# Optimization experiments

Hardware: AMD Instinct MI355X
Metric: run time of the kernel (lower is better)

The kernel has to match this reference:

```python
import jax, jax.numpy as jnp
import numpy as np

N_HEADS = 8; N_LEVELS = 4; T_WINDOW = 2; N_CURR = 4; N_TEMP = 2; D_MODEL = 256
D_HEAD = D_MODEL // N_HEADS
SHAPES = [[4, 32, 48], [4, 16, 24], [4, 8, 12], [4, 4, 6]]  # (T, H, W) per level
LEN_IN = sum(t * h * w for t, h, w in SHAPES)  # 8160
LEN_Q = LEN_IN
N_BATCH = 1


def _bilinear_sample(value_l, loc):
    # value_l: (N, M, H, W, D); loc: (N, M, Q, P, 2) normalized to [0, 1].
    # Matches torch grid_sample(mode='bilinear', padding_mode='zeros', align_corners=False)
    # with grid = 2*loc - 1, i.e. pixel coords x = loc_x*W - 0.5, y = loc_y*H - 0.5.
    N, M, H, W, D = value_l.shape
    Q, P = loc.shape[2], loc.shape[3]
    x = loc[..., 0] * W - 0.5
    y = loc[..., 1] * H - 0.5
    x0 = jnp.floor(x); y0 = jnp.floor(y)
    wx = x - x0; wy = y - y0
    flat = value_l.reshape(N, M, H * W, D)

    def gather(xi, yi):
        valid = ((xi >= 0) & (xi < W) & (yi >= 0) & (yi < H)).astype(value_l.dtype)
        idx = (jnp.clip(yi, 0, H - 1) * W + jnp.clip(xi, 0, W - 1)).astype(jnp.int32)
        g = jnp.take_along_axis(flat, idx.reshape(N, M, Q * P, 1), axis=2)
        return g.reshape(N, M, Q, P, D) * valid[..., None]

    v00 = gather(x0, y0); v10 = gather(x0 + 1.0, y0)
    v01 = gather(x0, y0 + 1.0); v11 = gather(x0 + 1.0, y0 + 1.0)
    return (v00 * ((1 - wx) * (1 - wy))[..., None] + v10 * (wx * (1 - wy))[..., None]
            + v01 * ((1 - wx) * wy)[..., None] + v11 * (wx * wy)[..., None])


def _forward(query, reference_points, temporal_offsets, input_flatten, shapes, starts,
             Wv, bv, Ws, bs, Wa, ba, Wts, bts, Wta, bta, Wo, bo):
    N, Lq, _ = query.shape
    value = (input_flatten @ Wv + bv).reshape(N, -1, N_HEADS, D_HEAD)
    ts_off = (query @ Wts + bts).reshape(N, Lq, N_HEADS, N_LEVELS, T_WINDOW, N_TEMP, 2)
    t_attn = (query @ Wta + bta).reshape(N, Lq, N_HEADS, N_LEVELS * T_WINDOW * N_TEMP)
    c_attn = (query @ Wa + ba).reshape(N, Lq, N_HEADS, N_LEVELS * N_CURR)
    # joint softmax over current + temporal sampling points (as in the source)
    attn = jax.nn.softmax(jnp.concatenate([c_attn, t_attn], axis=-1), axis=-1)
    aw_c = attn[..., :N_LEVELS * N_CURR].reshape(N, Lq, N_HEADS, N_LEVELS, N_CURR)
    aw_t = attn[..., N_LEVELS * N_CURR:].reshape(N, Lq, N_HEADS, N_LEVELS, T_WINDOW * N_TEMP)
    aw = jnp.concatenate([aw_c, aw_t], axis=4)  # (N, Lq, M, L, P)
    c_off = (query @ Ws + bs).reshape(N, Lq, N_HEADS, N_LEVELS, N_CURR, 2)
    # flattened-temporal grid per level: width W_l, height T_l*H_l
    norm = jnp.array([[w, t * h] for t, h, w in shapes], dtype=query.dtype)  # (L, 2)
    loc_c = reference_points[:, :, None, :, None, :] + c_off / norm[None, None, None, :, None, :]
    loc_t = (reference_points[:, :, None, :, None, None, :]
             + temporal_offsets[:, :, None, :, :, None, :]
             + ts_off / norm[None, None, None, :, None, None, :])
    loc_t = loc_t.reshape(N, Lq, N_HEADS, N_LEVELS, T_WINDOW * N_TEMP, 2)
    locs = jnp.concatenate([loc_c, loc_t], axis=4)  # (N, Lq, M, L, P, 2)
    out = jnp.zeros((N, N_HEADS, Lq, D_HEAD), query.dtype)
    for l, (t, h, w) in enumerate(shapes):
        s = starts[l]
        vl = value[:, s:s + t * h * w].transpose(0, 2, 1, 3).reshape(N, N_HEADS, t * h, w, D_HEAD)
        loc_l = locs[:, :, :, l].transpose(0, 2, 1, 3, 4)   # (N, M, Lq, P, 2)
        sampled = _bilinear_sample(vl, loc_l)               # (N, M, Lq, P, Dh)
        w_l = aw[:, :, :, l].transpose(0, 2, 1, 3)          # (N, M, Lq, P)
        out = out + jnp.einsum('nmqpd,nmqp->nmqd', sampled, w_l)
    out = out.transpose(0, 2, 1, 3).reshape(N, Lq, D_MODEL)
    return out @ Wo + bo


def setup_inputs() -> dict:
    key = jax.random.key(0)
    ks = jax.random.split(key, 18)
    D = D_MODEL
    sc = 0.02
    query = jax.random.normal(ks[0], (N_BATCH, LEN_Q, D), jnp.float32)
    reference_points = jax.random.uniform(ks[1], (N_BATCH, LEN_Q, N_LEVELS, 2), jnp.float32)
    temporal_offsets = jax.random.uniform(ks[2], (N_BATCH, LEN_Q, N_LEVELS, T_WINDOW, 2),
                                          jnp.float32, minval=-0.25, maxval=0.25)
    input_flatten = jax.random.normal(ks[3], (N_BATCH, LEN_IN, D), jnp.float32)
    input_spatial_shapes = jnp.array(SHAPES, dtype=jnp.int32)
    starts = np.cumsum([0] + [t * h * w for t, h, w in SHAPES])[:-1]
    input_level_start_index = jnp.array(starts, dtype=jnp.int32)
    n_off = N_HEADS * N_LEVELS * N_CURR * 2          # 256
    n_att = N_HEADS * N_LEVELS * N_CURR              # 128
    n_toff = N_HEADS * N_LEVELS * T_WINDOW * N_TEMP * 2  # 256
    n_tatt = N_HEADS * N_LEVELS * T_WINDOW * N_TEMP      # 128
    return {
        'query': query, 'reference_points': reference_points,
        'temporal_offsets': temporal_offsets, 'input_flatten': input_flatten,
        'input_spatial_shapes': input_spatial_shapes,
        'input_level_start_index': input_level_start_index,
        'Wv': jax.random.normal(ks[4], (D, D), jnp.float32) * sc,
        'bv': jnp.zeros((D,), jnp.float32),
        'Ws': jax.random.normal(ks[5], (D, n_off), jnp.float32) * sc,
        'bs': jax.random.normal(ks[6], (n_off,), jnp.float32) * 2.0,
        'Wa': jax.random.normal(ks[7], (D, n_att), jnp.float32) * sc,
        'ba': jnp.zeros((n_att,), jnp.float32),
        'Wts': jax.random.normal(ks[8], (D, n_toff), jnp.float32) * sc,
        'bts': jax.random.normal(ks[9], (n_toff,), jnp.float32) * 2.0,
        'Wta': jax.random.normal(ks[10], (D, n_tatt), jnp.float32) * sc,
        'bta': jnp.zeros((n_tatt,), jnp.float32),
        'Wo': jax.random.normal(ks[11], (D, D), jnp.float32) * sc,
        'bo': jnp.zeros((D,), jnp.float32),
    }


def reference(query, reference_points, temporal_offsets, input_flatten,
              input_spatial_shapes, input_level_start_index,
              Wv, bv, Ws, bs, Wa, ba, Wts, bts, Wta, bta, Wo, bo):
    shapes = [tuple(int(v) for v in row) for row in np.asarray(input_spatial_shapes)]
    starts = [int(v) for v in np.asarray(input_level_start_index)]
    return _forward(query, reference_points, temporal_offsets, input_flatten,
                    shapes, starts, Wv, bv, Ws, bs, Wa, ba, Wts, bts, Wta, bta, Wo, bo)
```

## Files before the change

kernel.cpp:

```cpp
#include <hip/hip_runtime.h>


#define LEN 8160
#define NCONV8 (2 * LEN * 256 / 8)
#define NPACK8 (1280 * 256 / 8)

typedef __attribute__((ext_vector_type(8))) short bf16x8;
typedef __attribute__((ext_vector_type(8))) unsigned short u16x8;
typedef __attribute__((ext_vector_type(4))) float f32x4;

__device__ __forceinline__ unsigned short rne_bf16(float v)
{
    unsigned u = __float_as_uint(v);
    return (unsigned short)((u + 0x7FFFu + ((u >> 16) & 1u)) >> 16);
}

__device__ __forceinline__ void split_bf16(float v, unsigned short* hi, unsigned short* lo)
{
    unsigned u = __float_as_uint(v);
    unsigned r = (u + 0x7FFFu + ((u >> 16) & 1u)) & 0xFFFF0000u;
    float hif = __uint_as_float(r);
    float lof = v - hif;
    unsigned ul = __float_as_uint(lof);
    unsigned rl = (ul + 0x7FFFu + ((ul >> 16) & 1u)) >> 16;
    *hi = (unsigned short)(r >> 16);
    *lo = (unsigned short)rl;
}

__device__ __forceinline__ float bf2f(unsigned short s)
{
    return __uint_as_float(((unsigned)s) << 16);
}

__global__ __launch_bounds__(256) void prep_kernel(
    const float* __restrict__ inpf, const float* __restrict__ query,
    const float* __restrict__ Ws, const float* __restrict__ bs,
    const float* __restrict__ Wa, const float* __restrict__ ba,
    const float* __restrict__ Wts, const float* __restrict__ bts,
    const float* __restrict__ Wta, const float* __restrict__ bta,
    const float* __restrict__ Wv, const float* __restrict__ Wo,
    unsigned short* __restrict__ Ahi, unsigned short* __restrict__ Alo,
    unsigned short* __restrict__ Qhi, unsigned short* __restrict__ Qlo,
    unsigned short* __restrict__ Whi, unsigned short* __restrict__ Wlo,
    float* __restrict__ bcat)
{
    int idx = blockIdx.x * 256 + threadIdx.x;
    if (idx < NCONV8) {
        int which = (idx >= NCONV8 / 2) ? 1 : 0;
        int off = (idx - which * (NCONV8 / 2)) * 8;
        const float* src = which ? query : inpf;
        float4 a = *(const float4*)(src + off);
        float4 b = *(const float4*)(src + off + 4);
        unsigned short h[8], l[8];
        split_bf16(a.x, &h[0], &l[0]); split_bf16(a.y, &h[1], &l[1]);
        split_bf16(a.z, &h[2], &l[2]); split_bf16(a.w, &h[3], &l[3]);
        split_bf16(b.x, &h[4], &l[4]); split_bf16(b.y, &h[5], &l[5]);
        split_bf16(b.z, &h[6], &l[6]); split_bf16(b.w, &h[7], &l[7]);
        uint4 hv, lv;
        hv.x = h[0] | ((unsigned)h[1] << 16); hv.y = h[2] | ((unsigned)h[3] << 16);
        hv.z = h[4] | ((unsigned)h[5] << 16); hv.w = h[6] | ((unsigned)h[7] << 16);
        lv.x = l[0] | ((unsigned)l[1] << 16); lv.y = l[2] | ((unsigned)l[3] << 16);
        lv.z = l[4] | ((unsigned)l[5] << 16); lv.w = l[6] | ((unsigned)l[7] << 16);
        if (which) { *(uint4*)(Qhi + off) = hv; *(uint4*)(Qlo + off) = lv; }
        else       { *(uint4*)(Ahi + off) = hv; *(uint4*)(Alo + off) = lv; }
    } else if (idx < NCONV8 + NPACK8) {
        int j8 = idx - NCONV8;
        int n = j8 >> 5;
        int k0 = (j8 & 31) << 3;
        unsigned short h[8], l[8];
        #pragma unroll
        for (int t = 0; t < 8; t++) {
            int k = k0 + t;
            float v;
            if (n < 256) v = Wv[k * 256 + n];
            else if (n < 1024) {
                int j = n - 256;
                if (j < 256)      v = Ws [k * 256 + j];
                else if (j < 384) v = Wa [k * 128 + (j - 256)];
                else if (j < 640) v = Wts[k * 256 + (j - 384)];
                else              v = Wta[k * 128 + (j - 640)];
            } else v = Wo[k * 256 + (n - 1024)];
            split_bf16(v, &h[t], &l[t]);
        }
        uint4 hv, lv;
        hv.x = h[0] | ((unsigned)h[1] << 16); hv.y = h[2] | ((unsigned)h[3] << 16);
        hv.z = h[4] | ((unsigned)h[5] << 16); hv.w = h[6] | ((unsigned)h[7] << 16);
        lv.x = l[0] | ((unsigned)l[1] << 16); lv.y = l[2] | ((unsigned)l[3] << 16);
        lv.z = l[4] | ((unsigned)l[5] << 16); lv.w = l[6] | ((unsigned)l[7] << 16);
        *(uint4*)(Whi + n * 256 + k0) = hv;
        *(uint4*)(Wlo + n * 256 + k0) = lv;
    } else if (idx < NCONV8 + NPACK8 + 768) {
        int j = idx - (NCONV8 + NPACK8);
        float v;
        if (j < 256)      v = bs[j];
        else if (j < 384) v = ba[j - 256];
        else if (j < 640) v = bts[j - 384];
        else              v = bta[j - 640];
        bcat[j] = v;
    }
}

__global__ __launch_bounds__(512) void gemm_mfma_dual(
    const unsigned short* __restrict__ A0hi, const unsigned short* __restrict__ A0lo,
    const unsigned short* __restrict__ B0hi, const unsigned short* __restrict__ B0lo,
    const float* __restrict__ bias0, void* __restrict__ C0, int N0, int mode0, int nbx0,
    const unsigned short* __restrict__ A1hi, const unsigned short* __restrict__ A1lo,
    const unsigned short* __restrict__ B1hi, const unsigned short* __restrict__ B1lo,
    const float* __restrict__ bias1, void* __restrict__ C1, int N1, int mode1)
{
    __shared__ unsigned short Bf[2 * 8 * 4 * 64 * 8];
    const int tid = threadIdx.x;
    const int wave = tid >> 6, lane = tid & 63;
    int bx = blockIdx.x;
    const int by = blockIdx.y;

    const unsigned short *Ahi, *Alo, *Bhi, *Blo;
    const float* bias; void* C; int N, mode;
    if (bx < nbx0) {
        Ahi = A0hi; Alo = A0lo; Bhi = B0hi; Blo = B0lo;
        bias = bias0; C = C0; N = N0; mode = mode0;
    } else {
        bx -= nbx0;
        Ahi = A1hi; Alo = A1lo; Bhi = B1hi; Blo = B1lo;
        bias = bias1; C = C1; N = N1; mode = mode1;
    }

    #pragma unroll
    for (int t = 0; t < 8; t++) {
        int f = t * 512 + tid;
        int ln = f & 63, nt = (f >> 6) & 3, kt = (f >> 8) & 7, pl = f >> 11;
        const unsigned short* src = (pl ? Blo : Bhi)
            + (size_t)(bx * 64 + nt * 16 + (ln & 15)) * 256 + kt * 32 + (ln >> 4) * 8;
        *(uint4*)(&Bf[(size_t)f * 8]) = *(const uint4*)src;
    }
    __syncthreads();

    const int lm = lane & 15;
    const int kq = lane >> 4;
    const int m0 = by * 256 + wave * 32 + lm;
    const unsigned short* aH0 = Ahi + (size_t)m0 * 256 + kq * 8;
    const unsigned short* aL0 = Alo + (size_t)m0 * 256 + kq * 8;

    f32x4 acc[2][4] = {};
    #pragma unroll
    for (int kt = 0; kt < 8; kt++) {
        bf16x8 ah0 = *(const bf16x8*)(aH0 + kt * 32);
        bf16x8 al0 = *(const bf16x8*)(aL0 + kt * 32);
        bf16x8 ah1 = *(const bf16x8*)(aH0 + 16 * 256 + kt * 32);
        bf16x8 al1 = *(const bf16x8*)(aL0 + 16 * 256 + kt * 32);
        #pragma unroll
        for (int nt = 0; nt < 4; nt++) {
            const int fb = (kt * 4 + nt) * 64 + lane;
            bf16x8 bh = *(const bf16x8*)(&Bf[(size_t)fb * 8]);
            bf16x8 bl = *(const bf16x8*)(&Bf[(size_t)(fb + 2048) * 8]);
            acc[0][nt] = __builtin_amdgcn_mfma_f32_16x16x32_bf16(ah0, bh, acc[0][nt], 0, 0, 0);
            acc[0][nt] = __builtin_amdgcn_mfma_f32_16x16x32_bf16(ah0, bl, acc[0][nt], 0, 0, 0);
            acc[0][nt] = __builtin_amdgcn_mfma_f32_16x16x32_bf16(al0, bh, acc[0][nt], 0, 0, 0);
            acc[1][nt] = __builtin_amdgcn_mfma_f32_16x16x32_bf16(ah1, bh, acc[1][nt], 0, 0, 0);
            acc[1][nt] = __builtin_amdgcn_mfma_f32_16x16x32_bf16(ah1, bl, acc[1][nt], 0, 0, 0);
            acc[1][nt] = __builtin_amdgcn_mfma_f32_16x16x32_bf16(al1, bh, acc[1][nt], 0, 0, 0);
        }
    }

    const int col = bx * 64 + lm;
    #pragma unroll
    for (int sub = 0; sub < 2; sub++) {
        const int row0 = by * 256 + wave * 32 + sub * 16 + kq * 4;
        #pragma unroll
        for (int nt = 0; nt < 4; nt++) {
            float bb = bias[col + nt * 16];
            #pragma unroll
            for (int r = 0; r < 4; r++) {
                int row = row0 + r;
                if (row < LEN) {
                    float v = acc[sub][nt][r] + bb;
                    if (mode) ((unsigned short*)C)[(size_t)row * N + col + nt * 16] = rne_bf16(v);
                    else      ((float*)C)[(size_t)row * N + col + nt * 16] = v;
                }
            }
        }
    }
}

__global__ __launch_bounds__(256) void sample_kernel(
    const unsigned short* __restrict__ value,
    const float* __restrict__ proj,
    const float* __restrict__ refp,
    const float* __restrict__ toff,
    unsigned short* __restrict__ attn_hi,
    unsigned short* __restrict__ attn_lo)
{
    const int q = blockIdx.x;
    const int head = threadIdx.x >> 5;
    const int lane = threadIdx.x & 31;
    __shared__ int4   s_idx[8][32];
    __shared__ float4 s_w[8][32];

    const float* p = proj + (size_t)q * 768;

    {
        const int i = lane;
        float logit, ox, oy, rx, ry;
        int l;
        if (i < 16) {
            l = i >> 2; int pt2 = i & 3;
            logit = p[256 + head * 16 + i];
            ox = p[head * 32 + l * 8 + pt2 * 2 + 0];
            oy = p[head * 32 + l * 8 + pt2 * 2 + 1];
            rx = refp[q * 8 + l * 2 + 0];
            ry = refp[q * 8 + l * 2 + 1];
        } else {
            int j = i - 16; l = j >> 2;
            int tp = j & 3, tw = tp >> 1, nt = tp & 1;
            logit = p[640 + head * 16 + j];
            ox = p[384 + head * 32 + l * 8 + tw * 4 + nt * 2 + 0];
            oy = p[384 + head * 32 + l * 8 + tw * 4 + nt * 2 + 1];
            rx = refp[q * 8 + l * 2 + 0] + toff[q * 16 + l * 4 + tw * 2 + 0];
            ry = refp[q * 8 + l * 2 + 1] + toff[q * 16 + l * 4 + tw * 2 + 1];
        }
        const int Wl = 48 >> l;
        const int Hgl = 128 >> l;
        const int st = 8192 - (8192 >> (2 * l));
        const float fW = (float)Wl, fHg = (float)Hgl;
        float x = (rx + ox / fW) * fW - 0.5f;
        float y = (ry + oy / fHg) * fHg - 0.5f;

        float mx = logit;
        #pragma unroll
        for (int off = 16; off > 0; off >>= 1)
            mx = fmaxf(mx, __shfl_xor(mx, off, 32));
        float e = expf(logit - mx);
        float s = e;
        #pragma unroll
        for (int off = 16; off > 0; off >>= 1)
            s += __shfl_xor(s, off, 32);
        float w = e / s;

        float fx = floorf(x), fy = floorf(y);
        float wx = x - fx, wy = y - fy;
        int x0 = (int)fx, y0 = (int)fy;
        int x1 = x0 + 1, y1 = y0 + 1;
        float m00 = ((unsigned)x0 < (unsigned)Wl && (unsigned)y0 < (unsigned)Hgl) ? 1.f : 0.f;
        float m10 = ((unsigned)x1 < (unsigned)Wl && (unsigned)y0 < (unsigned)Hgl) ? 1.f : 0.f;
        float m01 = ((unsigned)x0 < (unsigned)Wl && (unsigned)y1 < (unsigned)Hgl) ? 1.f : 0.f;
        float m11 = ((unsigned)x1 < (unsigned)Wl && (unsigned)y1 < (unsigned)Hgl) ? 1.f : 0.f;
        int cx0 = min(max(x0, 0), Wl - 1), cx1 = min(max(x1, 0), Wl - 1);
        int cy0 = min(max(y0, 0), Hgl - 1), cy1 = min(max(y1, 0), Hgl - 1);
        int4 ii;
        ii.x = (st + cy0 * Wl + cx0) * 512;
        ii.y = (st + cy0 * Wl + cx1) * 512;
        ii.z = (st + cy1 * Wl + cx0) * 512;
        ii.w = (st + cy1 * Wl + cx1) * 512;
        float sx0 = 1.f - wx, sy0 = 1.f - wy;
        float4 ww;
        ww.x = w * sx0 * sy0 * m00;
        ww.y = w * wx  * sy0 * m10;
        ww.z = w * sx0 * wy  * m01;
        ww.w = w * wx  * wy  * m11;
        s_idx[head][lane] = ii;
        s_w[head][lane] = ww;
    }
    __syncthreads();

    const int pt8 = lane >> 2;
    const int cg  = lane & 3;
    const char* vbase = (const char*)value + head * 64 + cg * 16;
    float acc[8] = {0.f, 0.f, 0.f, 0.f, 0.f, 0.f, 0.f, 0.f};
    #pragma unroll
    for (int i = 0; i < 4; i++) {
        int pidx = (i << 3) | pt8;
        int4 ii = s_idx[head][pidx];
        float4 ww = s_w[head][pidx];
        u16x8 v0 = *(const u16x8*)(vbase + ii.x);
        u16x8 v1 = *(const u16x8*)(vbase + ii.y);
        u16x8 v2 = *(const u16x8*)(vbase + ii.z);
        u16x8 v3 = *(const u16x8*)(vbase + ii.w);
        #pragma unroll
        for (int j = 0; j < 8; j++) {
            acc[j] = fmaf(ww.x, bf2f(v0[j]), acc[j]);
            acc[j] = fmaf(ww.y, bf2f(v1[j]), acc[j]);
            acc[j] = fmaf(ww.z, bf2f(v2[j]), acc[j]);
            acc[j] = fmaf(ww.w, bf2f(v3[j]), acc[j]);
        }
    }
    #pragma unroll
    for (int off = 4; off <= 16; off <<= 1)
        #pragma unroll
        for (int j = 0; j < 8; j++)
            acc[j] += __shfl_xor(acc[j], off, 32);

    if (pt8 == 0) {
        unsigned short h[8], l[8];
        #pragma unroll
        for (int j = 0; j < 8; j++) split_bf16(acc[j], &h[j], &l[j]);
        uint4 hv, lv;
        hv.x = h[0] | ((unsigned)h[1] << 16); hv.y = h[2] | ((unsigned)h[3] << 16);
        hv.z = h[4] | ((unsigned)h[5] << 16); hv.w = h[6] | ((unsigned)h[7] << 16);
        lv.x = l[0] | ((unsigned)l[1] << 16); lv.y = l[2] | ((unsigned)l[3] << 16);
        lv.z = l[4] | ((unsigned)l[5] << 16); lv.w = l[6] | ((unsigned)l[7] << 16);
        size_t o = (size_t)q * 256 + head * 32 + cg * 8;
        *(uint4*)(attn_hi + o) = hv;
        *(uint4*)(attn_lo + o) = lv;
    }
}

extern "C" void kernel_launch(void* const* d_in, const int* in_sizes, int n_in,
                              void* d_out, int out_size, void* d_ws, size_t ws_size,
                              hipStream_t stream)
{
    const float* query = (const float*)d_in[0];
    const float* refp  = (const float*)d_in[1];
    const float* toff  = (const float*)d_in[2];
    const float* inpf  = (const float*)d_in[3];
    const float* Wv  = (const float*)d_in[6];
    const float* bv  = (const float*)d_in[7];
    const float* Ws_ = (const float*)d_in[8];
    const float* bs_ = (const float*)d_in[9];
    const float* Wa  = (const float*)d_in[10];
    const float* ba  = (const float*)d_in[11];
    const float* Wts = (const float*)d_in[12];
    const float* bts = (const float*)d_in[13];
    const float* Wta = (const float*)d_in[14];
    const float* bta = (const float*)d_in[15];
    const float* Wo  = (const float*)d_in[16];
    const float* bo  = (const float*)d_in[17];
    float* out = (float*)d_out;

    unsigned short* value_bf = (unsigned short*)d_ws;
    float* proj = (float*)(value_bf + (size_t)LEN * 256);
    float* bcat = proj + (size_t)LEN * 768;
    unsigned short* Whi = (unsigned short*)(bcat + 768);
    unsigned short* Wlo = Whi + 1280 * 256;
    unsigned short* Ahi = Wlo + 1280 * 256;
    unsigned short* Alo = Ahi + (size_t)8192 * 256;
    unsigned short* Qhi = Alo + (size_t)8192 * 256;
    unsigned short* Qlo = Qhi + (size_t)8192 * 256;

    prep_kernel<<<2203, 256, 0, stream>>>(inpf, query, Ws_, bs_, Wa, ba,
                                          Wts, bts, Wta, bta, Wv, Wo,
                                          Ahi, Alo, Qhi, Qlo, Whi, Wlo, bcat);
    gemm_mfma_dual<<<dim3(16, 32), 512, 0, stream>>>(
        Ahi, Alo, Whi, Wlo, bv, value_bf, 256, 1, 4,
        Qhi, Qlo, Whi + 256 * 256, Wlo + 256 * 256, bcat, proj, 768, 0);
    sample_kernel<<<LEN, 256, 0, stream>>>(value_bf, proj, refp, toff, Ahi, Alo);
    gemm_mfma_dual<<<dim3(4, 32), 512, 0, stream>>>(
        Ahi, Alo, Whi + 1024 * 256, Wlo + 1024 * 256, bo, out, 256, 0, 4,
        Ahi, Alo, Whi + 1024 * 256, Wlo + 1024 * 256, bo, out, 256, 0);
}
```

Measured before the change: 184.9 us.

## Store value head-major and gather bilinear pairs with adjacent-column loads

```diff
diff --git a/kernel.cpp b/kernel.cpp
--- a/kernel.cpp
+++ b/kernel.cpp
@@ -100,7 +100,7 @@
     }
 }
 
-__global__ __launch_bounds__(512) void gemm_mfma_dual(
+__global__ __launch_bounds__(256) void gemm_mfma_dual(
     const unsigned short* __restrict__ A0hi, const unsigned short* __restrict__ A0lo,
     const unsigned short* __restrict__ B0hi, const unsigned short* __restrict__ B0lo,
     const float* __restrict__ bias0, void* __restrict__ C0, int N0, int mode0, int nbx0,
@@ -108,7 +108,7 @@
     const unsigned short* __restrict__ B1hi, const unsigned short* __restrict__ B1lo,
     const float* __restrict__ bias1, void* __restrict__ C1, int N1, int mode1)
 {
-    __shared__ unsigned short Bf[2 * 8 * 4 * 64 * 8];
+    __shared__ unsigned short Bf[2 * 4 * 4 * 64 * 8];
     const int tid = threadIdx.x;
     const int wave = tid >> 6, lane = tid & 63;
     int bx = blockIdx.x;
@@ -125,57 +125,67 @@
         bias = bias1; C = C1; N = N1; mode = mode1;
     }
 
-    #pragma unroll
-    for (int t = 0; t < 8; t++) {
-        int f = t * 512 + tid;
-        int ln = f & 63, nt = (f >> 6) & 3, kt = (f >> 8) & 7, pl = f >> 11;
-        const unsigned short* src = (pl ? Blo : Bhi)
-            + (size_t)(bx * 64 + nt * 16 + (ln & 15)) * 256 + kt * 32 + (ln >> 4) * 8;
-        *(uint4*)(&Bf[(size_t)f * 8]) = *(const uint4*)src;
-    }
-    __syncthreads();
-
     const int lm = lane & 15;
     const int kq = lane >> 4;
-    const int m0 = by * 256 + wave * 32 + lm;
-    const unsigned short* aH0 = Ahi + (size_t)m0 * 256 + kq * 8;
-    const unsigned short* aL0 = Alo + (size_t)m0 * 256 + kq * 8;
+    const int m0 = by * 128 + wave * 32 + lm;
+    const unsigned short* aHp = Ahi + (size_t)m0 * 256 + kq * 8;
+    const unsigned short* aLp = Alo + (size_t)m0 * 256 + kq * 8;
 
     f32x4 acc[2][4] = {};
     #pragma unroll
-    for (int kt = 0; kt < 8; kt++) {
-        bf16x8 ah0 = *(const bf16x8*)(aH0 + kt * 32);
-        bf16x8 al0 = *(const bf16x8*)(aL0 + kt * 32);
-        bf16x8 ah1 = *(const bf16x8*)(aH0 + 16 * 256 + kt * 32);
-        bf16x8 al1 = *(const bf16x8*)(aL0 + 16 * 256 + kt * 32);
-        #pragma unroll
-        for (int nt = 0; nt < 4; nt++) {
-            const int fb = (kt * 4 + nt) * 64 + lane;
-            bf16x8 bh = *(const bf16x8*)(&Bf[(size_t)fb * 8]);
-            bf16x8 bl = *(const bf16x8*)(&Bf[(size_t)(fb + 2048) * 8]);
-            acc[0][nt] = __builtin_amdgcn_mfma_f32_16x16x32_bf16(ah0, bh, acc[0][nt], 0, 0, 0);
-            acc[0][nt] = __builtin_amdgcn_mfma_f32_16x16x32_bf16(ah0, bl, acc[0][nt], 0, 0, 0);
-            acc[0][nt] = __builtin_amdgcn_mfma_f32_16x16x32_bf16(al0, bh, acc[0][nt], 0, 0, 0);
-            acc[1][nt] = __builtin_amdgcn_mfma_f32_16x16x32_bf16(ah1, bh, acc[1][nt], 0, 0, 0);
-            acc[1][nt] = __builtin_amdgcn_mfma_f32_16x16x32_bf16(ah1, bl, acc[1][nt], 0, 0, 0);
-            acc[1][nt] = __builtin_amdgcn_mfma_f32_16x16x32_bf16(al1, bh, acc[1][nt], 0, 0, 0);
-        }
+    for (int chunk = 0; chunk < 2; chunk++) {
+        #pragma unroll
+        for (int t = 0; t < 8; t++) {
+            int f = t * 256 + tid;
+            int ln = f & 63, nt = (f >> 6) & 3, kt = (f >> 8) & 3, pl = f >> 10;
+            const unsigned short* src = (pl ? Blo : Bhi)
+                + (size_t)(bx * 64 + nt * 16 + (ln & 15)) * 256
+                + chunk * 128 + kt * 32 + (ln >> 4) * 8;
+            *(uint4*)(&Bf[(size_t)f * 8]) = *(const uint4*)src;
+        }
+        __syncthreads();
+        #pragma unroll
+        for (int kt = 0; kt < 4; kt++) {
+            const int ko = chunk * 128 + kt * 32;
+            bf16x8 ah0 = *(const bf16x8*)(aHp + ko);
+            bf16x8 al0 = *(const bf16x8*)(aLp + ko);
+            bf16x8 ah1 = *(const bf16x8*)(aHp + 16 * 256 + ko);
+            bf16x8 al1 = *(const bf16x8*)(aLp + 16 * 256 + ko);
+            #pragma unroll
+            for (int nt = 0; nt < 4; nt++) {
+                const int fb = (kt * 4 + nt) * 64 + lane;
+                bf16x8 bh = *(const bf16x8*)(&Bf[(size_t)fb * 8]);
+                bf16x8 bl = *(const bf16x8*)(&Bf[(size_t)(fb + 1024) * 8]);
+                acc[0][nt] = __builtin_amdgcn_mfma_f32_16x16x32_bf16(ah0, bh, acc[0][nt], 0, 0, 0);
+                acc[0][nt] = __builtin_amdgcn_mfma_f32_16x16x32_bf16(ah0, bl, acc[0][nt], 0, 0, 0);
+                acc[0][nt] = __builtin_amdgcn_mfma_f32_16x16x32_bf16(al0, bh, acc[0][nt], 0, 0, 0);
+                acc[1][nt] = __builtin_amdgcn_mfma_f32_16x16x32_bf16(ah1, bh, acc[1][nt], 0, 0, 0);
+                acc[1][nt] = __builtin_amdgcn_mfma_f32_16x16x32_bf16(ah1, bl, acc[1][nt], 0, 0, 0);
+                acc[1][nt] = __builtin_amdgcn_mfma_f32_16x16x32_bf16(al1, bh, acc[1][nt], 0, 0, 0);
+            }
+        }
+        __syncthreads();
     }
 
     const int col = bx * 64 + lm;
     #pragma unroll
     for (int sub = 0; sub < 2; sub++) {
-        const int row0 = by * 256 + wave * 32 + sub * 16 + kq * 4;
+        const int row0 = by * 128 + wave * 32 + sub * 16 + kq * 4;
         #pragma unroll
         for (int nt = 0; nt < 4; nt++) {
-            float bb = bias[col + nt * 16];
+            int c = col + nt * 16;
+            float bb = bias[c];
             #pragma unroll
             for (int r = 0; r < 4; r++) {
                 int row = row0 + r;
                 if (row < LEN) {
                     float v = acc[sub][nt][r] + bb;
-                    if (mode) ((unsigned short*)C)[(size_t)row * N + col + nt * 16] = rne_bf16(v);
-                    else      ((float*)C)[(size_t)row * N + col + nt * 16] = v;
+                    if (mode) {
+                        ((unsigned short*)C)[(size_t)(c >> 5) * 8192 * 32
+                                             + (size_t)row * 32 + (c & 31)] = rne_bf16(v);
+                    } else {
+                        ((float*)C)[(size_t)row * N + c] = v;
+                    }
                 }
             }
         }
@@ -193,7 +203,7 @@
     const int q = blockIdx.x;
     const int head = threadIdx.x >> 5;
     const int lane = threadIdx.x & 31;
-    __shared__ int4   s_idx[8][32];
+    __shared__ int2   s_row[8][32];
     __shared__ float4 s_w[8][32];
 
     const float* p = proj + (size_t)q * 768;
@@ -240,47 +250,48 @@
         float wx = x - fx, wy = y - fy;
         int x0 = (int)fx, y0 = (int)fy;
         int x1 = x0 + 1, y1 = y0 + 1;
-        float m00 = ((unsigned)x0 < (unsigned)Wl && (unsigned)y0 < (unsigned)Hgl) ? 1.f : 0.f;
-        float m10 = ((unsigned)x1 < (unsigned)Wl && (unsigned)y0 < (unsigned)Hgl) ? 1.f : 0.f;
-        float m01 = ((unsigned)x0 < (unsigned)Wl && (unsigned)y1 < (unsigned)Hgl) ? 1.f : 0.f;
-        float m11 = ((unsigned)x1 < (unsigned)Wl && (unsigned)y1 < (unsigned)Hgl) ? 1.f : 0.f;
+        float mx0 = ((unsigned)x0 < (unsigned)Wl) ? 1.f : 0.f;
+        float mx1 = ((unsigned)x1 < (unsigned)Wl) ? 1.f : 0.f;
+        float my0 = ((unsigned)y0 < (unsigned)Hgl) ? 1.f : 0.f;
+        float my1 = ((unsigned)y1 < (unsigned)Hgl) ? 1.f : 0.f;
         int cx0 = min(max(x0, 0), Wl - 1), cx1 = min(max(x1, 0), Wl - 1);
         int cy0 = min(max(y0, 0), Hgl - 1), cy1 = min(max(y1, 0), Hgl - 1);
-        int4 ii;
-        ii.x = (st + cy0 * Wl + cx0) * 512;
-        ii.y = (st + cy0 * Wl + cx1) * 512;
-        ii.z = (st + cy1 * Wl + cx0) * 512;
-        ii.w = (st + cy1 * Wl + cx1) * 512;
+        int xb = min(max(x0, 0), Wl - 2);
         float sx0 = 1.f - wx, sy0 = 1.f - wy;
+        float aL = (cx0 == xb     ? sx0 * mx0 : 0.f) + (cx1 == xb     ? wx * mx1 : 0.f);
+        float aR = (cx0 == xb + 1 ? sx0 * mx0 : 0.f) + (cx1 == xb + 1 ? wx * mx1 : 0.f);
+        float by0 = sy0 * my0, by1 = wy * my1;
+        int2 rr;
+        rr.x = (st + cy0 * Wl + xb) * 64;
+        rr.y = (st + cy1 * Wl + xb) * 64;
         float4 ww;
-        ww.x = w * sx0 * sy0 * m00;
-        ww.y = w * wx  * sy0 * m10;
-        ww.z = w * sx0 * wy  * m01;
-        ww.w = w * wx  * wy  * m11;
-        s_idx[head][lane] = ii;
+        ww.x = w * aL * by0;
+        ww.y = w * aR * by0;
+        ww.z = w * aL * by1;
+        ww.w = w * aR * by1;
+        s_row[head][lane] = rr;
         s_w[head][lane] = ww;
     }
     __syncthreads();
 
-    const int pt8 = lane >> 2;
-    const int cg  = lane & 3;
-    const char* vbase = (const char*)value + head * 64 + cg * 16;
+    const int pt4  = lane >> 3;
+    const int half = (lane >> 2) & 1;
+    const int cg   = lane & 3;
+    const char* vbase = (const char*)value + head * (8192 * 64) + half * 64 + cg * 16;
     float acc[8] = {0.f, 0.f, 0.f, 0.f, 0.f, 0.f, 0.f, 0.f};
     #pragma unroll
-    for (int i = 0; i < 4; i++) {
-        int pidx = (i << 3) | pt8;
-        int4 ii = s_idx[head][pidx];
+    for (int i = 0; i < 8; i++) {
+        int pidx = (i << 2) | pt4;
+        int2 rr = s_row[head][pidx];
         float4 ww = s_w[head][pidx];
-        u16x8 v0 = *(const u16x8*)(vbase + ii.x);
-        u16x8 v1 = *(const u16x8*)(vbase + ii.y);
-        u16x8 v2 = *(const u16x8*)(vbase + ii.z);
-        u16x8 v3 = *(const u16x8*)(vbase + ii.w);
+        u16x8 v0 = *(const u16x8*)(vbase + rr.x);
+        u16x8 v1 = *(const u16x8*)(vbase + rr.y);
+        float w0 = half ? ww.y : ww.x;
+        float w1 = half ? ww.w : ww.z;
         #pragma unroll
         for (int j = 0; j < 8; j++) {
-            acc[j] = fmaf(ww.x, bf2f(v0[j]), acc[j]);
-            acc[j] = fmaf(ww.y, bf2f(v1[j]), acc[j]);
-            acc[j] = fmaf(ww.z, bf2f(v2[j]), acc[j]);
-            acc[j] = fmaf(ww.w, bf2f(v3[j]), acc[j]);
+            acc[j] = fmaf(w0, bf2f(v0[j]), acc[j]);
+            acc[j] = fmaf(w1, bf2f(v1[j]), acc[j]);
         }
     }
     #pragma unroll
@@ -289,7 +300,7 @@
         for (int j = 0; j < 8; j++)
             acc[j] += __shfl_xor(acc[j], off, 32);
 
-    if (pt8 == 0) {
+    if (lane < 4) {
         unsigned short h[8], l[8];
         #pragma unroll
         for (int j = 0; j < 8; j++) split_bf16(acc[j], &h[j], &l[j]);
@@ -327,7 +338,7 @@
     float* out = (float*)d_out;
 
     unsigned short* value_bf = (unsigned short*)d_ws;
-    float* proj = (float*)(value_bf + (size_t)LEN * 256);
+    float* proj = (float*)(value_bf + (size_t)8 * 8192 * 32);
     float* bcat = proj + (size_t)LEN * 768;
     unsigned short* Whi = (unsigned short*)(bcat + 768);
     unsigned short* Wlo = Whi + 1280 * 256;
@@ -339,11 +350,11 @@
     prep_kernel<<<2203, 256, 0, stream>>>(inpf, query, Ws_, bs_, Wa, ba,
                                           Wts, bts, Wta, bta, Wv, Wo,
                                           Ahi, Alo, Qhi, Qlo, Whi, Wlo, bcat);
-    gemm_mfma_dual<<<dim3(16, 32), 512, 0, stream>>>(
+    gemm_mfma_dual<<<dim3(16, 64), 256, 0, stream>>>(
         Ahi, Alo, Whi, Wlo, bv, value_bf, 256, 1, 4,
         Qhi, Qlo, Whi + 256 * 256, Wlo + 256 * 256, bcat, proj, 768, 0);
     sample_kernel<<<LEN, 256, 0, stream>>>(value_bf, proj, refp, toff, Ahi, Alo);
-    gemm_mfma_dual<<<dim3(4, 32), 512, 0, stream>>>(
+    gemm_mfma_dual<<<dim3(4, 64), 256, 0, stream>>>(
         Ahi, Alo, Whi + 1024 * 256, Wlo + 1024 * 256, bo, out, 256, 0, 4,
         Ahi, Alo, Whi + 1024 * 256, Wlo + 1024 * 256, bo, out, 256, 0);
 }
```

Result: no change. 186.9 us (+1.0%).
